# Optimization experiments

Measured on AMD Instinct MI355X. Metric: run time of the kernel, lower is better.

Reference implementation:

```python
import jax, jax.numpy as jnp
import numpy as np

WIN_SIZE = 400
WIN_SHIFT = 160
BATCH = 32
T = 480000

def povey_window(n):
    # Kaldi default 'povey' window: (0.5 - 0.5*cos(2*pi*k/(n-1)))**0.85
    k = np.arange(n, dtype=np.float64)
    w = (0.5 - 0.5 * np.cos(2.0 * np.pi * k / (n - 1))) ** 0.85
    return jnp.asarray(w, dtype=jnp.float32)

def setup_inputs() -> dict:
    key = jax.random.key(0)
    x = jax.random.normal(key, (BATCH, T), dtype=jnp.float32)
    window = povey_window(WIN_SIZE)
    return {"x": x, "window": window, "win_shift": WIN_SHIFT}

def reference(x, window, win_shift):
    # Equivalent to conv1d with diagonal weight window[k]*eye(win_size):
    # out[b, k, f] = window[k] * x[b, f*win_shift + k]
    win_size = window.shape[0]
    n_frames = (x.shape[-1] - win_size) // win_shift + 1
    starts = jnp.arange(n_frames) * win_shift               # [F]
    idx = starts[:, None] + jnp.arange(win_size)[None, :]   # [F, W]
    frames = x[:, idx]                                      # [B, F, W]
    out = frames * window                                   # broadcast over W
    return jnp.transpose(out, (0, 2, 1))                    # [B, W, F]
```

## Files before the change

### kernel.cpp

```cpp
#include <hip/hip_runtime.h>

#define WIN_SIZE   400
#define WIN_SHIFT  160
#define BATCH      32
#define T_LEN      480000
#define NFRAMES    2998
#define WCHUNK     16
#define NWC        (WIN_SIZE / WCHUNK)
#define NBLOCKS    (BATCH * NWC)
#define PER_XCD    (NBLOCKS / 8)
#define FCHUNK     256
#define NITER      12
#define TAILF      (NFRAMES - (NITER-1)*FCHUNK)
#define LBUF       4128

typedef float f32x2 __attribute__((ext_vector_type(2)));

__device__ __forceinline__ int swz(int a) { return a ^ ((a >> 5) & 31); }

__global__ __launch_bounds__(256) void window_frame_kernel(
    const float* __restrict__ x, const float* __restrict__ window,
    float* __restrict__ out)
{
    __shared__ float ls[2][LBUF];
    __shared__ float lw[WCHUNK];

    const int flat = blockIdx.x;
    const int lin  = (flat & 7) * PER_XCD + (flat >> 3);
    const int b    = lin / NWC;
    const int w0   = (lin % NWC) * WCHUNK;

    const int tid  = threadIdx.x;
    const int lane = tid & 63;
    const int wid  = tid >> 6;

    if (tid < WCHUNK) lw[tid] = window[w0 + tid];

    const float* __restrict__ xb = x + (long)b * T_LEN + w0;

    float4 pf[4];
    #pragma unroll
    for (int p = 0; p < 4; ++p) {
        int t = tid + 256 * p;
        pf[p] = *(const float4*)(xb + (long)(t >> 2) * WIN_SHIFT + 4 * (t & 3));
    }

    for (int it = 0; it < NITER; ++it) {
        float* buf = ls[it & 1];
        const int f0 = it * FCHUNK;
        const int nf = (it == NITER - 1) ? TAILF : FCHUNK;

        #pragma unroll
        for (int p = 0; p < 4; ++p) {
            int t = tid + 256 * p;
            int frl = t >> 2;
            if (frl < nf) {
                float4 v = pf[p];
                int a = 16 * frl + 4 * (t & 3);
                buf[swz(a + 0)] = v.x;
                buf[swz(a + 1)] = v.y;
                buf[swz(a + 2)] = v.z;
                buf[swz(a + 3)] = v.w;
            }
        }
        __syncthreads();

        if (it + 1 < NITER) {
            const int nf2 = (it + 1 == NITER - 1) ? TAILF : FCHUNK;
            const float* __restrict__ xn = xb + (long)(f0 + FCHUNK) * WIN_SHIFT;
            #pragma unroll
            for (int p = 0; p < 4; ++p) {
                int t = tid + 256 * p;
                int frl = t >> 2;
                if (frl < nf2)
                    pf[p] = *(const float4*)(xn + (long)frl * WIN_SHIFT + 4 * (t & 3));
            }
        }

        #pragma unroll
        for (int c = 0; c < 4; ++c) {
            const int i = 4 * wid + c;
            const float wv = lw[i];
            float* __restrict__ orow =
                out + ((long)(b * WIN_SIZE + w0 + i)) * NFRAMES + f0;
            #pragma unroll
            for (int s = 0; s < 2; ++s) {
                int fl = 2 * lane + 128 * s;
                if (fl < nf) {
                    f32x2 v;
                    v.x = buf[swz(16 * fl + i)]        * wv;
                    v.y = buf[swz(16 * (fl + 1) + i)]  * wv;
                    *(f32x2*)(orow + fl) = v;
                }
            }
        }
    }
}

extern "C" void kernel_launch(void* const* d_in, const int* in_sizes, int n_in,
                              void* d_out, int out_size, void* d_ws, size_t ws_size,
                              hipStream_t stream) {
    const float* x      = (const float*)d_in[0];
    const float* window = (const float*)d_in[1];
    float* out = (float*)d_out;

    window_frame_kernel<<<NBLOCKS, 256, 0, stream>>>(x, window, out);
}
```

Measured before the change: 45.94 us.

## Reuse each loaded input column across overlapping windows sharing shift residue

Each block now loads 8 sample columns per 160-sample segment and emits every output row whose window offset shares that residue modulo the shift: 24 rows for the first 80 residues, 16 for the rest. Each frame group of 510 frames is staged once in LDS. The aim is to remove the roughly 2.5x redundant global reads of x caused by overlapping windows. In exchange, the grid shrinks from 800 to 640 blocks, per-block work becomes uneven (24 vs 16 rows), and the row loop is no longer fully unrolled.

```diff
diff --git a/kernel.cpp b/kernel.cpp
--- a/kernel.cpp
+++ b/kernel.cpp
@@ -5,14 +5,14 @@
 #define BATCH      32
 #define T_LEN      480000
 #define NFRAMES    2998
-#define WCHUNK     16
-#define NWC        (WIN_SIZE / WCHUNK)
-#define NBLOCKS    (BATCH * NWC)
+#define RCHUNK     8
+#define NRC        20
+#define NBLOCKS    (BATCH * NRC)
 #define PER_XCD    (NBLOCKS / 8)
-#define FCHUNK     256
-#define NITER      12
-#define TAILF      (NFRAMES - (NITER-1)*FCHUNK)
-#define LBUF       4128
+#define NG         510
+#define SF         512
+#define NITER      6
+#define LBUF       (SF * RCHUNK + 32)
 
 typedef float f32x2 __attribute__((ext_vector_type(2)));
 
@@ -23,40 +23,40 @@
     float* __restrict__ out)
 {
     __shared__ float ls[2][LBUF];
-    __shared__ float lw[WCHUNK];
+    __shared__ float lw[24];
 
     const int flat = blockIdx.x;
     const int lin  = (flat & 7) * PER_XCD + (flat >> 3);
-    const int b    = lin / NWC;
-    const int w0   = (lin % NWC) * WCHUNK;
+    const int b    = lin / NRC;
+    const int rc   = lin % NRC;
+    const int r0   = rc * RCHUNK;
+    const int nrows = (r0 < 80) ? 24 : 16;
 
-    const int tid  = threadIdx.x;
-    const int lane = tid & 63;
-    const int wid  = tid >> 6;
+    const int tid = threadIdx.x;
+    if (tid < nrows)
+        lw[tid] = window[r0 + (tid & 7) + WIN_SHIFT * (tid >> 3)];
 
-    if (tid < WCHUNK) lw[tid] = window[w0 + tid];
-
-    const float* __restrict__ xb = x + (long)b * T_LEN + w0;
+    const float* __restrict__ xb = x + (long)b * T_LEN + r0;
 
     float4 pf[4];
     #pragma unroll
     for (int p = 0; p < 4; ++p) {
-        int t = tid + 256 * p;
-        pf[p] = *(const float4*)(xb + (long)(t >> 2) * WIN_SHIFT + 4 * (t & 3));
+        int i4 = tid + 256 * p;
+        pf[p] = *(const float4*)(xb + (long)(i4 >> 1) * WIN_SHIFT + 4 * (i4 & 1));
     }
 
     for (int it = 0; it < NITER; ++it) {
         float* buf = ls[it & 1];
-        const int f0 = it * FCHUNK;
-        const int nf = (it == NITER - 1) ? TAILF : FCHUNK;
+        const int g0     = it * NG;
+        const int sAvail = min(SF, 3000 - g0);
+        const int nf     = min(NG, NFRAMES - g0);
 
         #pragma unroll
         for (int p = 0; p < 4; ++p) {
-            int t = tid + 256 * p;
-            int frl = t >> 2;
-            if (frl < nf) {
+            int i4 = tid + 256 * p;
+            if ((i4 >> 1) < sAvail) {
                 float4 v = pf[p];
-                int a = 16 * frl + 4 * (t & 3);
+                int a = 4 * i4;
                 buf[swz(a + 0)] = v.x;
                 buf[swz(a + 1)] = v.y;
                 buf[swz(a + 2)] = v.z;
@@ -66,30 +66,32 @@
         __syncthreads();
 
         if (it + 1 < NITER) {
-            const int nf2 = (it + 1 == NITER - 1) ? TAILF : FCHUNK;
-            const float* __restrict__ xn = xb + (long)(f0 + FCHUNK) * WIN_SHIFT;
+            const int g0n  = g0 + NG;
+            const int sAv2 = min(SF, 3000 - g0n);
+            const float* __restrict__ xn = xb + (long)g0n * WIN_SHIFT;
             #pragma unroll
             for (int p = 0; p < 4; ++p) {
-                int t = tid + 256 * p;
-                int frl = t >> 2;
-                if (frl < nf2)
-                    pf[p] = *(const float4*)(xn + (long)frl * WIN_SHIFT + 4 * (t & 3));
+                int i4 = tid + 256 * p;
+                if ((i4 >> 1) < sAv2)
+                    pf[p] = *(const float4*)(xn + (long)(i4 >> 1) * WIN_SHIFT + 4 * (i4 & 1));
             }
         }
 
-        #pragma unroll
-        for (int c = 0; c < 4; ++c) {
-            const int i = 4 * wid + c;
+        const int lane = tid & 63;
+        const int wid  = tid >> 6;
+        for (int i = wid; i < nrows; i += 4) {
+            const int rr = i & 7, j = i >> 3;
+            const int w  = r0 + rr + WIN_SHIFT * j;
             const float wv = lw[i];
             float* __restrict__ orow =
-                out + ((long)(b * WIN_SIZE + w0 + i)) * NFRAMES + f0;
+                out + ((long)(b * WIN_SIZE + w)) * NFRAMES + g0;
             #pragma unroll
-            for (int s = 0; s < 2; ++s) {
+            for (int s = 0; s < 4; ++s) {
                 int fl = 2 * lane + 128 * s;
                 if (fl < nf) {
                     f32x2 v;
-                    v.x = buf[swz(16 * fl + i)]        * wv;
-                    v.y = buf[swz(16 * (fl + 1) + i)]  * wv;
+                    v.x = buf[swz(8 * (fl + j)     + rr)] * wv;
+                    v.y = buf[swz(8 * (fl + 1 + j) + rr)] * wv;
                     *(f32x2*)(orow + fl) = v;
                 }
             }
```

New measurement: 41.41 us. 1.11x faster.
